# Optimization experiments

Hardware: AMD Instinct MI355X
Metric: run time of the kernel (lower is better)

Reference implementation:

```python
import jax, jax.numpy as jnp
import numpy as np

INF = 1e12  # constant.INFINITY_NUMBER in the original repo
NEG = -1e30  # stand-in for -inf in masked softmax (grad-safe)


def pool_max(h, mask):
    # h: [B,S,D], mask: [B,S,1] bool (True = masked out)
    return jnp.max(jnp.where(mask, -INF, h), axis=1)


def setup_inputs() -> dict:
    key = jax.random.key(0)
    B, S, V = 512, 128, 50000
    D_EMB, D_POS, D_NER, D_DEP = 300, 30, 30, 100
    HID = 300
    IN = D_EMB + D_POS + D_NER  # 360
    NPOS, NNER, NDEP, NCLS = 54, 23, 42, 42
    ks = jax.random.split(key, 16)
    words = jax.random.randint(ks[0], (B, S), 1, V)
    pos = jax.random.randint(ks[1], (B, S), 1, NPOS)
    ner = jax.random.randint(ks[2], (B, S), 1, NNER)
    deprel = jax.random.randint(ks[3], (B, S), 1, NDEP)
    # random dependency tree: head of token t is a random earlier token; token 0 is root
    rng = np.random.default_rng(0)
    heads = np.zeros((B, S), dtype=np.int64)
    for t in range(1, S):
        heads[:, t] = rng.integers(0, t, size=B)
    adj_np = np.zeros((B, S, S), dtype=np.float32)
    bi = np.arange(B)[:, None]
    ti = np.arange(1, S)[None, :]
    adj_np[bi, heads[:, 1:], np.broadcast_to(ti, (B, S - 1))] = 1.0  # directed head->dep, no self-loop
    adj = jnp.asarray(adj_np)
    # subj at position 5, obj at position 20 (subj_pos/obj_pos are relative offsets; ==0 marks entity)
    subj_pos = (jnp.broadcast_to(jnp.arange(S), (B, S)) - 5).astype(jnp.int32)
    obj_pos = (jnp.broadcast_to(jnp.arange(S), (B, S)) - 20).astype(jnp.int32)

    def p(k, shape, scale=0.02):
        return jax.random.normal(k, shape, jnp.float32) * scale

    return dict(
        words=words, pos=pos, ner=ner, deprel=deprel,
        subj_pos=subj_pos, obj_pos=obj_pos, adj=adj,
        emb_w=p(ks[4], (V, D_EMB)),
        pos_w=p(ks[5], (NPOS, D_POS)),
        ner_w=p(ks[6], (NNER, D_NER)),
        dep_w=p(ks[7], (NDEP, D_DEP)),
        attn_w=p(ks[8], (D_DEP, IN), 0.001),  # Attention.weight ~ N(0, 0.001)
        W0=p(ks[9], (IN, HID)), b0=jnp.zeros((HID,), jnp.float32),
        W1=p(ks[10], (HID, HID)), b1=jnp.zeros((HID,), jnp.float32),
        mlp0_w=p(ks[11], (3 * HID, HID)), mlp0_b=jnp.zeros((HID,), jnp.float32),
        mlp1_w=p(ks[12], (HID, HID)), mlp1_b=jnp.zeros((HID,), jnp.float32),
        cls_w=p(ks[13], (HID, NCLS)), cls_b=jnp.zeros((NCLS,), jnp.float32),
    )


def reference(words, pos, ner, deprel, subj_pos, obj_pos, adj,
              emb_w, pos_w, ner_w, dep_w, attn_w,
              W0, b0, W1, b1, mlp0_w, mlp0_b, mlp1_w, mlp1_b, cls_w, cls_b):
    # embeddings -> [B,S,360]
    h = jnp.concatenate([emb_w[words], pos_w[pos], ner_w[ner]], axis=2)
    denom = jnp.sum(adj, axis=2, keepdims=True) + 1.0  # [B,S,1]
    pool_mask = ((jnp.sum(adj, axis=2) + jnp.sum(adj, axis=1)) == 0)[:, :, None]  # [B,S,1]
    d_mask = jnp.sum(adj, axis=1) == 0  # [B,S] (in-degree zero)
    # deprel attention -> edge weights
    dep_e = jnp.where(d_mask[:, :, None], 0.0, dep_w[deprel])  # [B,S,Ddep]
    query = pool_max(h, pool_mask)  # [B,360]
    scores = jnp.einsum('bsd,de,be->bs', dep_e, attn_w, query)
    scores = jnp.where(d_mask, NEG, scores)
    weights = jax.nn.softmax(scores, axis=1)  # [B,S]
    a = adj * weights[:, :, None]
    a = a + jnp.swapaxes(a, 1, 2)  # symmetrize
    # GCN layers: AxW = W(Ax) + W(h) => (Ax+h)@W + 2b, degree-normalized, ReLU
    for W, b in ((W0, b0), (W1, b1)):
        Ax = jnp.einsum('bst,btd->bsd', a, h)
        h = jax.nn.relu(((Ax + h) @ W + 2.0 * b) / denom)
    subj_mask = (subj_pos != 0)[:, :, None]
    obj_mask = (obj_pos != 0)[:, :, None]
    h_out = pool_max(h, pool_mask)
    subj_out = pool_max(h, subj_mask)
    obj_out = pool_max(h, obj_mask)
    out = jnp.concatenate([h_out, subj_out, obj_out], axis=1)  # [B,900]
    out = jax.nn.relu(out @ mlp0_w + mlp0_b)
    out = jax.nn.relu(out @ mlp1_w + mlp1_b)
    logits = out @ cls_w + cls_b
    return logits, h_out
```

## Files before the change

kernel.cpp:

```cpp
#include <hip/hip_runtime.h>
#include <cstdint>

typedef __bf16 bf16;
typedef bf16 bf16x8 __attribute__((ext_vector_type(8)));
typedef float f32x4 __attribute__((ext_vector_type(4)));

#define NB 512
#define SS 128
#define DIN 360
#define DINP 384
#define DHID 300
#define DHP 320
#define DDEPW 100
#define NCLS 42
#define KCAT 928

constexpr float INF_ = 1e12f;
constexpr float NEG_ = -1e30f;

__device__ __forceinline__ void gload16(const void* g, void* l) {
  __builtin_amdgcn_global_load_lds((const __attribute__((address_space(1))) void*)g,
                                   (__attribute__((address_space(3))) void*)l, 16, 0, 0);
}

__global__ void k_degrees(const float* __restrict__ adj, float* __restrict__ denom,
                          int* __restrict__ pmask, int* __restrict__ dmask) {
  int b = blockIdx.x, t = threadIdx.x;
  const float* A = adj + (size_t)b * SS * SS;
  float indeg = 0.f;
  for (int s = 0; s < SS; ++s) indeg += A[s * SS + t];
  float outdeg = 0.f;
  const float4* row = (const float4*)(A + t * SS);
#pragma unroll
  for (int i = 0; i < SS / 4; ++i) { float4 v = row[i]; outdeg += v.x + v.y + v.z + v.w; }
  int idx = b * SS + t;
  denom[idx] = outdeg + 1.f;
  pmask[idx] = ((indeg + outdeg) == 0.f) ? 1 : 0;
  dmask[idx] = (indeg == 0.f) ? 1 : 0;
}

__global__ void k_embed(const int* __restrict__ words, const int* __restrict__ pos,
                        const int* __restrict__ ner,
                        const float* __restrict__ emb_w, const float* __restrict__ pos_w,
                        const float* __restrict__ ner_w, bf16* __restrict__ h) {
  int tid = threadIdx.x;
  int tok0 = blockIdx.x * 16;
  for (int i = 0; i < 16; ++i) {
    int tok = tok0 + i;
    if (tid < 180) {
      int c = tid * 2;
      float2 v;
      if (c < 300)      v = *(const float2*)(emb_w + (size_t)words[tok] * 300 + c);
      else if (c < 330) v = *(const float2*)(pos_w + (size_t)pos[tok] * 30 + (c - 300));
      else              v = *(const float2*)(ner_w + (size_t)ner[tok] * 30 + (c - 330));
      union { bf16 b[2]; uint32_t u; } cvt;
      cvt.b[0] = (bf16)v.x; cvt.b[1] = (bf16)v.y;
      *(uint32_t*)(h + (size_t)tok * DINP + c) = cvt.u;
    } else {
      int c = 360 + (tid - 180) * 2;
      *(uint32_t*)(h + (size_t)tok * DINP + c) = 0u;
    }
  }
}

__global__ void k_prepw(const float* __restrict__ W, int K, int N,
                        bf16* __restrict__ WT, int RP, int SP) {
  int idx = blockIdx.x * 256 + threadIdx.x;
  if (idx >= RP * SP) return;
  int r = idx / SP, c = idx % SP;
  float v = (r < N && c < K) ? W[(size_t)c * N + r] : 0.f;
  WT[(size_t)r * SP + c] = (bf16)v;
}

__global__ void k_prepwb(const float* __restrict__ W, int K, int N,
                         bf16* __restrict__ WT, int KP, int NP) {
  int idx = blockIdx.x * 256 + threadIdx.x;
  if (idx >= NP * KP) return;
  int n = idx / KP, k = idx - n * KP;
  float v = (n < N && k < K) ? W[(size_t)k * N + n] : 0.f;
  WT[(size_t)n * KP + k] = (bf16)v;
}

__global__ void k_query_qa(const bf16* __restrict__ h, const int* __restrict__ pmask,
                           const float* __restrict__ attn_w, float* __restrict__ qa) {
  __shared__ float q[DIN];
  __shared__ int pm[SS];
  int b = blockIdx.x, tid = threadIdx.x;
  if (tid < SS) pm[tid] = pmask[b * SS + tid];
  __syncthreads();
  if (tid < DIN) {
    float m = -INF_;
    const bf16* hb = h + (size_t)b * SS * DINP + tid;
    for (int s = 0; s < SS; ++s) { float v = (float)hb[(size_t)s * DINP]; if (!pm[s]) m = fmaxf(m, v); }
    q[tid] = m;
  }
  __syncthreads();
  if (tid < DDEPW) {
    const float* wr = attn_w + (size_t)tid * DIN;
    float acc = 0.f;
    for (int e = 0; e < DIN; ++e) acc += wr[e] * q[e];
    qa[b * SS + tid] = acc;
  }
}

__global__ void k_weights(const int* __restrict__ deprel, const float* __restrict__ dep_w,
                          const int* __restrict__ dmask, const float* __restrict__ qa,
                          float* __restrict__ wts) {
  __shared__ float qs[DDEPW];
  __shared__ float red[SS];
  int b = blockIdx.x, s = threadIdx.x;
  if (s < DDEPW) qs[s] = qa[b * SS + s];
  __syncthreads();
  float score;
  if (dmask[b * SS + s]) score = NEG_;
  else {
    const float* dr = dep_w + (size_t)deprel[b * SS + s] * DDEPW;
    float acc = 0.f;
    for (int d = 0; d < DDEPW; ++d) acc += dr[d] * qs[d];
    score = acc;
  }
  red[s] = score; __syncthreads();
  for (int off = 64; off > 0; off >>= 1) { if (s < off) red[s] = fmaxf(red[s], red[s + off]); __syncthreads(); }
  float mx = red[0]; __syncthreads();
  float ex = expf(score - mx);
  red[s] = ex; __syncthreads();
  for (int off = 64; off > 0; off >>= 1) { if (s < off) red[s] += red[s + off]; __syncthreads(); }
  wts[b * SS + s] = ex / red[0];
}

__global__ void k_symmetrize(const float* __restrict__ adj, const float* __restrict__ wts,
                             bf16* __restrict__ amat) {
  __shared__ float tile[SS * SS];
  int b = blockIdx.x, tid = threadIdx.x;
  const float* Ab = adj + (size_t)b * SS * SS;
  bf16* ab = amat + (size_t)b * SS * SS;
#pragma unroll 4
  for (int i = 0; i < 64; ++i) {
    int idx = i * 256 + tid;
    int s_ = idx >> 7, t_ = idx & 127;
    tile[(s_ << 7) + ((t_ + s_) & 127)] = Ab[idx];
  }
  __syncthreads();
  const float* wb = wts + b * SS;
#pragma unroll 4
  for (int i = 0; i < 64; ++i) {
    int idx = i * 256 + tid;
    int s_ = idx >> 7, t_ = idx & 127;
    float v = tile[(s_ << 7) + ((t_ + s_) & 127)] * wb[s_]
            + tile[(t_ << 7) + ((s_ + t_) & 127)] * wb[t_];
    ab[idx] = (bf16)v;
  }
}

__global__ __launch_bounds__(256) void k_ah(
    const bf16* __restrict__ amat, const bf16* __restrict__ h,
    int SH, int NVALID, bf16* __restrict__ t, int ST) {
  __shared__ __align__(16) bf16 Xs[128 * 136];
  __shared__ __align__(16) bf16 Ys[32 * 136];
  int z = blockIdx.y;
  int nblk = blockIdx.x * 128;
  int tid = threadIdx.x;
  const bf16* Az = amat + (size_t)z * SS * SS;
  const bf16* hz = h + (size_t)z * SS * SH;
  {
    int c8 = (tid & 15) * 8;
#pragma unroll
    for (int it = 0; it < 8; ++it) {
      int r = it * 16 + (tid >> 4);
      *(bf16x8*)&Xs[r * 136 + c8] = *(const bf16x8*)&Az[r * SS + c8];
    }
  }
  int wid = tid >> 6, lane = tid & 63;
  int wm = (wid >> 1) * 64, wn = (wid & 1) * 64;
  int lr = lane & 15, lg = lane >> 4;
  f32x4 acc[4][4];
#pragma unroll
  for (int i = 0; i < 4; ++i)
#pragma unroll
    for (int j = 0; j < 4; ++j) acc[i][j] = (f32x4){0.f, 0.f, 0.f, 0.f};

  for (int k0 = 0; k0 < SS; k0 += 32) {
    {
      int c8 = (tid & 15) * 8;
      int col = nblk + c8;
#pragma unroll
      for (int it = 0; it < 2; ++it) {
        int r = it * 16 + (tid >> 4);
        bf16x8 v;
        if (col < SH) v = *(const bf16x8*)&hz[(size_t)(k0 + r) * SH + col];
        else { union { uint32_t u[4]; bf16x8 bv; } zz; zz.u[0]=zz.u[1]=zz.u[2]=zz.u[3]=0u; v = zz.bv; }
        *(bf16x8*)&Ys[r * 136 + c8] = v;
      }
    }
    __syncthreads();
    bf16x8 a[4], b[4];
#pragma unroll
    for (int mi = 0; mi < 4; ++mi)
      a[mi] = *(const bf16x8*)&Xs[(wm + mi * 16 + lr) * 136 + k0 + lg * 8];
#pragma unroll
    for (int nf = 0; nf < 4; ++nf) {
      bf16x8 bv;
#pragma unroll
      for (int i = 0; i < 8; ++i) bv[i] = Ys[(lg * 8 + i) * 136 + wn + nf * 16 + lr];
      b[nf] = bv;
    }
#pragma unroll
    for (int mi = 0; mi < 4; ++mi)
#pragma unroll
      for (int nf = 0; nf < 4; ++nf)
        acc[mi][nf] = __builtin_amdgcn_mfma_f32_16x16x32_bf16(a[mi], b[nf], acc[mi][nf], 0, 0, 0);
    __syncthreads();
  }
#pragma unroll
  for (int mi = 0; mi < 4; ++mi) {
    int m = wm + mi * 16 + lg * 4;
#pragma unroll
    for (int nf = 0; nf < 4; ++nf) {
      int n = nblk + wn + nf * 16 + lr;
      if (n < ST) {
#pragma unroll
        for (int i = 0; i < 4; ++i) {
          float v = (n < NVALID) ? (acc[mi][nf][i] + (float)hz[(size_t)(m + i) * SH + n]) : 0.f;
          t[((size_t)z * SS + m + i) * ST + n] = (bf16)v;
        }
      }
    }
  }
}

template<bool F32OUT>
__global__ __launch_bounds__(256, 4) void k_dense(
    const bf16* __restrict__ X, const bf16* __restrict__ Y,
    const float* __restrict__ bias, const float* __restrict__ denom,
    void* __restrict__ Cout, int K, int NVALID, int SC) {
  __shared__ __align__(16) bf16 As[128 * 64];
  __shared__ __align__(16) bf16 Bs[160 * 64];
  int tid = threadIdx.x;
  int mblk = blockIdx.y * 128, nblk = blockIdx.x * 160;
  int wid = tid >> 6, lane = tid & 63;
  int wm = (wid >> 1) * 64, wn = (wid & 1) * 80;
  int lr = lane & 15, lg = lane >> 4;
  int srow = tid >> 3, slot = tid & 7;
  f32x4 acc[4][5];
#pragma unroll
  for (int i = 0; i < 4; ++i)
#pragma unroll
    for (int j = 0; j < 5; ++j) acc[i][j] = (f32x4){0.f, 0.f, 0.f, 0.f};

  for (int k0 = 0; k0 < K; k0 += 64) {
    __syncthreads();
#pragma unroll
    for (int it = 0; it < 4; ++it) {
      int row = it * 32 + srow;
      int kg = slot ^ (row & 7);
      gload16(&X[(size_t)(mblk + row) * K + k0 + kg * 8], &As[(it * 256 + wid * 64) * 8]);
    }
#pragma unroll
    for (int it = 0; it < 5; ++it) {
      int row = it * 32 + srow;
      int kg = slot ^ (row & 7);
      gload16(&Y[(size_t)(nblk + row) * K + k0 + kg * 8], &Bs[(it * 256 + wid * 64) * 8]);
    }
    __syncthreads();
#pragma unroll
    for (int kk = 0; kk < 2; ++kk) {
      bf16x8 a[4], b[5];
#pragma unroll
      for (int mi = 0; mi < 4; ++mi) {
        int r = wm + mi * 16 + lr;
        a[mi] = *(const bf16x8*)&As[r * 64 + (((kk * 4 + lg) ^ (lr & 7)) * 8)];
      }
#pragma unroll
      for (int nf = 0; nf < 5; ++nf) {
        int r = wn + nf * 16 + lr;
        b[nf] = *(const bf16x8*)&Bs[r * 64 + (((kk * 4 + lg) ^ (lr & 7)) * 8)];
      }
#pragma unroll
      for (int mi = 0; mi < 4; ++mi)
#pragma unroll
        for (int nf = 0; nf < 5; ++nf)
          acc[mi][nf] = __builtin_amdgcn_mfma_f32_16x16x32_bf16(a[mi], b[nf], acc[mi][nf], 0, 0, 0);
    }
  }
#pragma unroll
  for (int mi = 0; mi < 4; ++mi) {
    int m0 = mblk + wm + mi * 16 + lg * 4;
    float dn[4];
#pragma unroll
    for (int i = 0; i < 4; ++i) dn[i] = denom[m0 + i];
#pragma unroll
    for (int nf = 0; nf < 5; ++nf) {
      int n = nblk + wn + nf * 16 + lr;
      if (n < NVALID) {
        float bs = 2.f * bias[n];
#pragma unroll
        for (int i = 0; i < 4; ++i) {
          float v = fmaxf((acc[mi][nf][i] + bs) / dn[i], 0.f);
          if (F32OUT) ((float*)Cout)[(size_t)(m0 + i) * SC + n] = v;
          else ((bf16*)Cout)[(size_t)(m0 + i) * SC + n] = (bf16)v;
        }
      }
    }
  }
}

template<bool RELU, bool BF16OUT, int KP, int NP, int NVALID>
__global__ __launch_bounds__(256) void k_mlp_mfma(
    const bf16* __restrict__ A, const bf16* __restrict__ BT,
    const float* __restrict__ bias, void* __restrict__ C, int M, int SC) {
  constexpr int NT = NP / 16;
  int wid = threadIdx.x >> 6, lane = threadIdx.x & 63;
  int wti = blockIdx.x * 4 + wid;
  int mt = wti / NT, nt = wti - mt * NT;
  if (mt * 16 >= M) return;
  int lr = lane & 15, lg = lane >> 4;
  const bf16* Ap = A + (size_t)(mt * 16 + lr) * KP + lg * 8;
  const bf16* Bp = BT + (size_t)(nt * 16 + lr) * KP + lg * 8;
  f32x4 acc = (f32x4){0.f, 0.f, 0.f, 0.f};
#pragma unroll
  for (int k0 = 0; k0 < KP; k0 += 32) {
    bf16x8 a = *(const bf16x8*)(Ap + k0);
    bf16x8 b = *(const bf16x8*)(Bp + k0);
    acc = __builtin_amdgcn_mfma_f32_16x16x32_bf16(a, b, acc, 0, 0, 0);
  }
  int n = nt * 16 + lr;
  int m0 = mt * 16 + lg * 4;
  float bs = (n < NVALID) ? bias[n] : 0.f;
  if (BF16OUT) {
#pragma unroll
    for (int i = 0; i < 4; ++i) {
      float v = 0.f;
      if (n < NVALID) { v = acc[i] + bs; if (RELU) v = fmaxf(v, 0.f); }
      ((bf16*)C)[(size_t)(m0 + i) * SC + n] = (bf16)v;
    }
  } else {
    if (n < NVALID) {
#pragma unroll
      for (int i = 0; i < 4; ++i) {
        float v = acc[i] + bs;
        if (RELU) v = fmaxf(v, 0.f);
        ((float*)C)[(size_t)(m0 + i) * SC + n] = v;
      }
    }
  }
}

__global__ void k_pool(const float* __restrict__ h, const int* __restrict__ pmask,
                       const int* __restrict__ subj_pos, const int* __restrict__ obj_pos,
                       bf16* __restrict__ catb, float* __restrict__ hout) {
  __shared__ int pm[SS], sm[SS], om[SS];
  int b = blockIdx.x, e = threadIdx.x;
  if (e < SS) {
    pm[e] = pmask[b * SS + e];
    sm[e] = (subj_pos[b * SS + e] != 0) ? 1 : 0;
    om[e] = (obj_pos[b * SS + e] != 0) ? 1 : 0;
  }
  __syncthreads();
  if (e < DHID) {
    const float* hb = h + (size_t)b * SS * DHID + e;
    float mh = -INF_, ms = -INF_, mo = -INF_;
    for (int s = 0; s < SS; ++s) {
      float v = hb[(size_t)s * DHID];
      if (!pm[s]) mh = fmaxf(mh, v);
      if (!sm[s]) ms = fmaxf(ms, v);
      if (!om[s]) mo = fmaxf(mo, v);
    }
    catb[(size_t)b * KCAT + e] = (bf16)mh;
    catb[(size_t)b * KCAT + 300 + e] = (bf16)ms;
    catb[(size_t)b * KCAT + 600 + e] = (bf16)mo;
    hout[(size_t)b * DHID + e] = mh;
  } else if (e < DHID + (KCAT - 3 * DHID)) {
    catb[(size_t)b * KCAT + 600 + e] = (bf16)0.f;
  }
}

extern "C" void kernel_launch(void* const* d_in, const int* in_sizes, int n_in,
                              void* d_out, int out_size, void* d_ws, size_t ws_size,
                              hipStream_t stream) {
  const int* words = (const int*)d_in[0];
  const int* pos = (const int*)d_in[1];
  const int* ner = (const int*)d_in[2];
  const int* deprel = (const int*)d_in[3];
  const int* subj_pos = (const int*)d_in[4];
  const int* obj_pos = (const int*)d_in[5];
  const float* adj = (const float*)d_in[6];
  const float* emb_w = (const float*)d_in[7];
  const float* pos_w = (const float*)d_in[8];
  const float* ner_w = (const float*)d_in[9];
  const float* dep_w = (const float*)d_in[10];
  const float* attn_w = (const float*)d_in[11];
  const float* W0 = (const float*)d_in[12];
  const float* b0 = (const float*)d_in[13];
  const float* W1 = (const float*)d_in[14];
  const float* b1 = (const float*)d_in[15];
  const float* mlp0_w = (const float*)d_in[16];
  const float* mlp0_b = (const float*)d_in[17];
  const float* mlp1_w = (const float*)d_in[18];
  const float* mlp1_b = (const float*)d_in[19];
  const float* cls_w = (const float*)d_in[20];
  const float* cls_b = (const float*)d_in[21];
  float* out = (float*)d_out;

  char* w = (char*)d_ws;
  bf16* h0 = (bf16*)w;
  bf16* h1 = (bf16*)w;
  float* h2f = (float*)w;
  w += 78643200;
  bf16* t1 = (bf16*)w;
  bf16* t2 = (bf16*)w;
  w += 50331648;
  bf16* amat = (bf16*)w; w += 16777216;
  bf16* W0T = (bf16*)w; w += 294912;
  bf16* W1T = (bf16*)w; w += 204800;
  float* denom = (float*)w; w += 262144;
  int* pmask = (int*)w; w += 262144;
  int* dmask = (int*)w; w += 262144;
  float* qa = (float*)w; w += 262144;
  float* wts = (float*)w; w += 262144;
  bf16* catb = (bf16*)w; w += 950272;
  bf16* m0b = (bf16*)w; w += 327680;
  bf16* m1b = (bf16*)w; w += 327680;
  bf16* M0T = (bf16*)w; w += 593920;
  bf16* M1T = (bf16*)w; w += 204800;
  bf16* CLT = (bf16*)w; w += 30720;

  k_prepw<<<(384 * 384 + 255) / 256, 256, 0, stream>>>(W0, DIN, DHID, W0T, DINP, DINP);
  k_prepw<<<(320 * 320 + 255) / 256, 256, 0, stream>>>(W1, DHID, DHID, W1T, DHP, DHP);
  k_prepwb<<<(320 * 928 + 255) / 256, 256, 0, stream>>>(mlp0_w, 900, DHID, M0T, KCAT, DHP);
  k_prepwb<<<(320 * 320 + 255) / 256, 256, 0, stream>>>(mlp1_w, DHID, DHID, M1T, DHP, DHP);
  k_prepwb<<<(48 * 320 + 255) / 256, 256, 0, stream>>>(cls_w, DHID, NCLS, CLT, DHP, 48);
  k_degrees<<<NB, SS, 0, stream>>>(adj, denom, pmask, dmask);
  k_embed<<<(NB * SS) / 16, 192, 0, stream>>>(words, pos, ner, emb_w, pos_w, ner_w, h0);
  k_query_qa<<<NB, 384, 0, stream>>>(h0, pmask, attn_w, qa);
  k_weights<<<NB, SS, 0, stream>>>(deprel, dep_w, dmask, qa, wts);
  k_symmetrize<<<NB, 256, 0, stream>>>(adj, wts, amat);

  k_ah<<<dim3(3, NB), 256, 0, stream>>>(amat, h0, DINP, DINP, t1, DINP);
  k_dense<false><<<dim3(2, NB), 256, 0, stream>>>(t1, W0T, b0, denom, h1, DINP, DHID, DHP);
  k_ah<<<dim3(3, NB), 256, 0, stream>>>(amat, h1, DHP, DHID, t2, DHP);
  k_dense<true><<<dim3(2, NB), 256, 0, stream>>>(t2, W1T, b1, denom, h2f, DHP, DHID, DHID);

  k_pool<<<NB, 384, 0, stream>>>(h2f, pmask, subj_pos, obj_pos, catb, out + NB * NCLS);

  k_mlp_mfma<true, true, KCAT, DHP, DHID><<<(512 / 16) * (DHP / 16) / 4, 256, 0, stream>>>(
      catb, M0T, mlp0_b, m0b, NB, DHP);
  k_mlp_mfma<true, true, DHP, DHP, DHID><<<(512 / 16) * (DHP / 16) / 4, 256, 0, stream>>>(
      m0b, M1T, mlp1_b, m1b, NB, DHP);
  k_mlp_mfma<false, false, DHP, 48, NCLS><<<(512 / 16) * (48 / 16) / 4, 256, 0, stream>>>(
      m1b, CLT, cls_b, out, NB, NCLS);
}
```

Baseline: 469.7 us.

## Reassociate GCN layer as A(hW)+hW and fuse epilogue into adjacency matmul

Each GCN layer used to compute (A·h + h) and then multiply by W. It now computes g = h·W first and then applies A·g + g, with bias, degree normalization and ReLU fused into the adjacency kernel. The intermediate is narrower (320 instead of 384 columns for the first layer), so the adjacency matmul and the intermediate buffer shrink. The adjacency kernel also loads the whole A and g tiles once, using swizzled LDS layouts and async global-to-LDS loads, instead of looping over K in chunks. The trade-offs are larger LDS use, which may lower occupancy, and an extra rounding of hW to bf16 before aggregation.

```diff
diff --git a/kernel.cpp b/kernel.cpp
--- a/kernel.cpp
+++ b/kernel.cpp
@@ -152,87 +152,9 @@
   }
 }
 
-__global__ __launch_bounds__(256) void k_ah(
-    const bf16* __restrict__ amat, const bf16* __restrict__ h,
-    int SH, int NVALID, bf16* __restrict__ t, int ST) {
-  __shared__ __align__(16) bf16 Xs[128 * 136];
-  __shared__ __align__(16) bf16 Ys[32 * 136];
-  int z = blockIdx.y;
-  int nblk = blockIdx.x * 128;
-  int tid = threadIdx.x;
-  const bf16* Az = amat + (size_t)z * SS * SS;
-  const bf16* hz = h + (size_t)z * SS * SH;
-  {
-    int c8 = (tid & 15) * 8;
-#pragma unroll
-    for (int it = 0; it < 8; ++it) {
-      int r = it * 16 + (tid >> 4);
-      *(bf16x8*)&Xs[r * 136 + c8] = *(const bf16x8*)&Az[r * SS + c8];
-    }
-  }
-  int wid = tid >> 6, lane = tid & 63;
-  int wm = (wid >> 1) * 64, wn = (wid & 1) * 64;
-  int lr = lane & 15, lg = lane >> 4;
-  f32x4 acc[4][4];
-#pragma unroll
-  for (int i = 0; i < 4; ++i)
-#pragma unroll
-    for (int j = 0; j < 4; ++j) acc[i][j] = (f32x4){0.f, 0.f, 0.f, 0.f};
-
-  for (int k0 = 0; k0 < SS; k0 += 32) {
-    {
-      int c8 = (tid & 15) * 8;
-      int col = nblk + c8;
-#pragma unroll
-      for (int it = 0; it < 2; ++it) {
-        int r = it * 16 + (tid >> 4);
-        bf16x8 v;
-        if (col < SH) v = *(const bf16x8*)&hz[(size_t)(k0 + r) * SH + col];
-        else { union { uint32_t u[4]; bf16x8 bv; } zz; zz.u[0]=zz.u[1]=zz.u[2]=zz.u[3]=0u; v = zz.bv; }
-        *(bf16x8*)&Ys[r * 136 + c8] = v;
-      }
-    }
-    __syncthreads();
-    bf16x8 a[4], b[4];
-#pragma unroll
-    for (int mi = 0; mi < 4; ++mi)
-      a[mi] = *(const bf16x8*)&Xs[(wm + mi * 16 + lr) * 136 + k0 + lg * 8];
-#pragma unroll
-    for (int nf = 0; nf < 4; ++nf) {
-      bf16x8 bv;
-#pragma unroll
-      for (int i = 0; i < 8; ++i) bv[i] = Ys[(lg * 8 + i) * 136 + wn + nf * 16 + lr];
-      b[nf] = bv;
-    }
-#pragma unroll
-    for (int mi = 0; mi < 4; ++mi)
-#pragma unroll
-      for (int nf = 0; nf < 4; ++nf)
-        acc[mi][nf] = __builtin_amdgcn_mfma_f32_16x16x32_bf16(a[mi], b[nf], acc[mi][nf], 0, 0, 0);
-    __syncthreads();
-  }
-#pragma unroll
-  for (int mi = 0; mi < 4; ++mi) {
-    int m = wm + mi * 16 + lg * 4;
-#pragma unroll
-    for (int nf = 0; nf < 4; ++nf) {
-      int n = nblk + wn + nf * 16 + lr;
-      if (n < ST) {
-#pragma unroll
-        for (int i = 0; i < 4; ++i) {
-          float v = (n < NVALID) ? (acc[mi][nf][i] + (float)hz[(size_t)(m + i) * SH + n]) : 0.f;
-          t[((size_t)z * SS + m + i) * ST + n] = (bf16)v;
-        }
-      }
-    }
-  }
-}
-
-template<bool F32OUT>
 __global__ __launch_bounds__(256, 4) void k_dense(
     const bf16* __restrict__ X, const bf16* __restrict__ Y,
-    const float* __restrict__ bias, const float* __restrict__ denom,
-    void* __restrict__ Cout, int K, int NVALID, int SC) {
+    bf16* __restrict__ Cout, int K, int SC) {
   __shared__ __align__(16) bf16 As[128 * 64];
   __shared__ __align__(16) bf16 Bs[160 * 64];
   int tid = threadIdx.x;
@@ -285,19 +207,104 @@
 #pragma unroll
   for (int mi = 0; mi < 4; ++mi) {
     int m0 = mblk + wm + mi * 16 + lg * 4;
-    float dn[4];
-#pragma unroll
-    for (int i = 0; i < 4; ++i) dn[i] = denom[m0 + i];
 #pragma unroll
     for (int nf = 0; nf < 5; ++nf) {
       int n = nblk + wn + nf * 16 + lr;
-      if (n < NVALID) {
-        float bs = 2.f * bias[n];
-#pragma unroll
-        for (int i = 0; i < 4; ++i) {
-          float v = fmaxf((acc[mi][nf][i] + bs) / dn[i], 0.f);
-          if (F32OUT) ((float*)Cout)[(size_t)(m0 + i) * SC + n] = v;
-          else ((bf16*)Cout)[(size_t)(m0 + i) * SC + n] = (bf16)v;
+#pragma unroll
+      for (int i = 0; i < 4; ++i)
+        Cout[(size_t)(m0 + i) * SC + n] = (bf16)acc[mi][nf][i];
+    }
+  }
+}
+
+template<bool F32OUT>
+__global__ __launch_bounds__(256) void k_ah(
+    const bf16* __restrict__ amat, const bf16* __restrict__ g,
+    const float* __restrict__ bias, const float* __restrict__ denom,
+    void* __restrict__ Hout, int SG, int NVALID, int SC) {
+  __shared__ __align__(16) bf16 Xs[128 * 128];
+  __shared__ __align__(16) bf16 Ys[160 * 128];
+  int z = blockIdx.y;
+  int nblk = blockIdx.x * 160;
+  int tid = threadIdx.x;
+  const bf16* Az = amat + (size_t)z * SS * SS;
+  const bf16* gz = g + (size_t)z * SS * SG;
+  {
+    int wv = tid >> 6;
+#pragma unroll
+    for (int it = 0; it < 8; ++it) {
+      int j = it * 256 + tid;
+      int row = j >> 4, slot = j & 15;
+      int kg = slot ^ (row & 15);
+      gload16(&Az[(size_t)row * SS + kg * 8], &Xs[(it * 256 + wv * 64) * 8]);
+    }
+  }
+  {
+    int m = tid & 127, half = tid >> 7;
+    int mg = m >> 3, ml = m & 7;
+#pragma unroll
+    for (int it = 0; it < 10; ++it) {
+      int n0 = (it * 2 + half) * 8;
+      bf16x8 v = *(const bf16x8*)&gz[(size_t)m * SG + nblk + n0];
+#pragma unroll
+      for (int j = 0; j < 8; ++j) {
+        int n = n0 + j;
+        Ys[n * 128 + ((mg ^ (n & 15)) * 8) + ml] = v[j];
+      }
+    }
+  }
+  __syncthreads();
+
+  int wid = tid >> 6, lane = tid & 63;
+  int wm = (wid >> 1) * 64, wn = (wid & 1) * 80;
+  int lr = lane & 15, lg = lane >> 4;
+  f32x4 acc[4][5];
+#pragma unroll
+  for (int i = 0; i < 4; ++i)
+#pragma unroll
+    for (int j = 0; j < 5; ++j) acc[i][j] = (f32x4){0.f, 0.f, 0.f, 0.f};
+
+#pragma unroll
+  for (int ks = 0; ks < 4; ++ks) {
+    int kg = ks * 4 + lg;
+    bf16x8 a[4], b[5];
+#pragma unroll
+    for (int mi = 0; mi < 4; ++mi) {
+      int r = wm + mi * 16 + lr;
+      a[mi] = *(const bf16x8*)&Xs[r * 128 + ((kg ^ (r & 15)) * 8)];
+    }
+#pragma unroll
+    for (int nf = 0; nf < 5; ++nf) {
+      int n = wn + nf * 16 + lr;
+      b[nf] = *(const bf16x8*)&Ys[n * 128 + ((kg ^ (n & 15)) * 8)];
+    }
+#pragma unroll
+    for (int mi = 0; mi < 4; ++mi)
+#pragma unroll
+      for (int nf = 0; nf < 5; ++nf)
+        acc[mi][nf] = __builtin_amdgcn_mfma_f32_16x16x32_bf16(a[mi], b[nf], acc[mi][nf], 0, 0, 0);
+  }
+
+#pragma unroll
+  for (int mi = 0; mi < 4; ++mi) {
+    int m0 = wm + mi * 16 + lg * 4;
+    float dn[4];
+#pragma unroll
+    for (int i = 0; i < 4; ++i) dn[i] = denom[z * SS + m0 + i];
+#pragma unroll
+    for (int nf = 0; nf < 5; ++nf) {
+      int n = wn + nf * 16 + lr;
+      int ng = nblk + n;
+      float bs = (ng < DHID) ? 2.f * bias[ng] : 0.f;
+#pragma unroll
+      for (int i = 0; i < 4; ++i) {
+        int m = m0 + i;
+        float gv = (float)Ys[n * 128 + (((m >> 3) ^ (n & 15)) * 8) + (m & 7)];
+        float v = fmaxf((acc[mi][nf][i] + gv + bs) / dn[i], 0.f);
+        if (F32OUT) {
+          if (ng < NVALID) ((float*)Hout)[((size_t)z * SS + m) * SC + ng] = v;
+        } else {
+          ((bf16*)Hout)[((size_t)z * SS + m) * SC + ng] = (bf16)v;
         }
       }
     }
@@ -406,9 +413,7 @@
   bf16* h1 = (bf16*)w;
   float* h2f = (float*)w;
   w += 78643200;
-  bf16* t1 = (bf16*)w;
-  bf16* t2 = (bf16*)w;
-  w += 50331648;
+  bf16* g = (bf16*)w; w += 41943040;
   bf16* amat = (bf16*)w; w += 16777216;
   bf16* W0T = (bf16*)w; w += 294912;
   bf16* W1T = (bf16*)w; w += 204800;
@@ -435,10 +440,10 @@
   k_weights<<<NB, SS, 0, stream>>>(deprel, dep_w, dmask, qa, wts);
   k_symmetrize<<<NB, 256, 0, stream>>>(adj, wts, amat);
 
-  k_ah<<<dim3(3, NB), 256, 0, stream>>>(amat, h0, DINP, DINP, t1, DINP);
-  k_dense<false><<<dim3(2, NB), 256, 0, stream>>>(t1, W0T, b0, denom, h1, DINP, DHID, DHP);
-  k_ah<<<dim3(3, NB), 256, 0, stream>>>(amat, h1, DHP, DHID, t2, DHP);
-  k_dense<true><<<dim3(2, NB), 256, 0, stream>>>(t2, W1T, b1, denom, h2f, DHP, DHID, DHID);
+  k_dense<<<dim3(2, NB), 256, 0, stream>>>(h0, W0T, g, DINP, DHP);
+  k_ah<false><<<dim3(2, NB), 256, 0, stream>>>(amat, g, b0, denom, h1, DHP, DHP, DHP);
+  k_dense<<<dim3(2, NB), 256, 0, stream>>>(h1, W1T, g, DHP, DHP);
+  k_ah<true><<<dim3(2, NB), 256, 0, stream>>>(amat, g, b1, denom, h2f, DHP, DHID, DHID);
 
   k_pool<<<NB, 384, 0, stream>>>(h2f, pmask, subj_pos, obj_pos, catb, out + NB * NCLS);
 
```

After: 432.5 us. 1.09x faster.
